# Kernel optimization log

Hardware: AMD Instinct MI355X
Metric: run time of the kernel (lower is better)

## Reference

```python
import jax, jax.numpy as jnp
import numpy as np

BN_EPS = 1e-5

def _binarize(x):
    # sign with STE semantics (Binarize on .data in torch => identity grad)
    b = jnp.where(x >= 0, 1.0, -1.0).astype(x.dtype)
    return x + jax.lax.stop_gradient(b - x)

def _bin_linear(x, w, b, binarize_input):
    xb = _binarize(x) if binarize_input else x
    wb = _binarize(w)
    return xb @ wb.T + b

def _bn(x, g, be, m, v):
    return (x - m) * (g * jax.lax.rsqrt(v + BN_EPS)) + be

def _hardtanh(x):
    return jnp.clip(x, -1.0, 1.0)

def setup_inputs() -> dict:
    key = jax.random.key(0)
    ks = jax.random.split(key, 8)
    B, D_in, H, D_out = 16384, 784, 4096, 10
    inp = {
        'x':  jax.random.normal(ks[0], (B, D_in), jnp.float32),
        'w1': jax.random.normal(ks[1], (H, D_in), jnp.float32) * 0.05,
        'b1': jax.random.normal(ks[2], (H,), jnp.float32) * 0.05,
        'g1': jnp.ones((H,), jnp.float32), 'be1': jnp.zeros((H,), jnp.float32),
        'm1': jnp.zeros((H,), jnp.float32), 'v1': jnp.ones((H,), jnp.float32),
        'w2': jax.random.normal(ks[3], (H, H), jnp.float32) * 0.05,
        'b2': jax.random.normal(ks[4], (H,), jnp.float32) * 0.05,
        'g2': jnp.ones((H,), jnp.float32), 'be2': jnp.zeros((H,), jnp.float32),
        'm2': jnp.zeros((H,), jnp.float32), 'v2': jnp.ones((H,), jnp.float32),
        'w3': jax.random.normal(ks[5], (H, H), jnp.float32) * 0.05,
        'b3': jax.random.normal(ks[6], (H,), jnp.float32) * 0.05,
        'g3': jnp.ones((H,), jnp.float32), 'be3': jnp.zeros((H,), jnp.float32),
        'm3': jnp.zeros((H,), jnp.float32), 'v3': jnp.ones((H,), jnp.float32),
        'w4': jax.random.normal(ks[7], (D_out, H), jnp.float32) * 0.05,
        'b4': jnp.zeros((D_out,), jnp.float32),
    }
    return inp

def reference(x, w1, b1, g1, be1, m1, v1,
              w2, b2, g2, be2, m2, v2,
              w3, b3, g3, be3, m3, v3,
              w4, b4):
    # eval mode: BN uses running stats, dropout is identity
    h = _bin_linear(x.reshape(-1, w1.shape[1]), w1, b1, binarize_input=False)
    h = _hardtanh(_bn(h, g1, be1, m1, v1))
    h = _bin_linear(h, w2, b2, binarize_input=True)
    h = _hardtanh(_bn(h, g2, be2, m2, v2))
    h = _bin_linear(h, w3, b3, binarize_input=True)
    h = _hardtanh(_bn(h, g3, be3, m3, v3))
    h = _bin_linear(h, w4, b4, binarize_input=True)
    return jax.nn.log_softmax(h, axis=1)
```

## Files before the change

kernel.cpp:

```cpp
#include <hip/hip_runtime.h>
#include <hip/hip_bf16.h>
#include <stdint.h>
#include <math.h>

#define BATCH 16384
#define DIN   784
#define HID   4096
#define DOUT  10
#define KW    128
#define KP    1600
#define CAP   1048576
#define BN_EPS 1e-5
#define TAU   0.05f

constexpr size_t SZ_BITS   = (size_t)BATCH * KW * 4;
constexpr size_t OFF_BITS1 = 0;
constexpr size_t OFF_BITS2 = OFF_BITS1 + SZ_BITS;
constexpr size_t OFF_W2B   = OFF_BITS2 + SZ_BITS;
constexpr size_t OFF_W3B   = OFF_W2B + (size_t)HID * KW * 4;
constexpr size_t OFF_W4B   = OFF_W3B + (size_t)HID * KW * 4;
constexpr size_t OFF_CNT   = OFF_W4B + 8192;
constexpr size_t OFF_LIST  = OFF_CNT + 256;
constexpr size_t OFF_XHL   = (OFF_LIST + (size_t)CAP * 4 + 255) & ~(size_t)255;
constexpr size_t OFF_WSD   = OFF_XHL + (size_t)BATCH * KP * 2;

typedef __attribute__((ext_vector_type(8))) short frag8;
typedef __attribute__((ext_vector_type(4))) float f32x4;

typedef const __attribute__((address_space(1))) uint32_t guint;
typedef __attribute__((address_space(3))) uint32_t luint;

__device__ __forceinline__ void load16_to_lds(const void* g, void* l) {
  __builtin_amdgcn_global_load_lds((guint*)g, (luint*)l, 16, 0, 0);
}

__device__ __forceinline__ unsigned short f2bf_bits(float x) {
  __hip_bfloat16 h = __float2bfloat16(x);
  return *reinterpret_cast<unsigned short*>(&h);
}
__device__ __forceinline__ float bf2f(unsigned short b) {
  union { unsigned int u; float f; } c;
  c.u = ((unsigned int)b) << 16;
  return c.f;
}

__global__ void zero_cnt_kernel(int* cnt) {
  if (threadIdx.x == 0) *cnt = 0;
}

__global__ __launch_bounds__(256) void binarize_kernel(
    const float* __restrict__ w, uint32_t* __restrict__ bits, int nwords) {
  int t = blockIdx.x * 256 + threadIdx.x;
  if (t >= nwords) return;
  const float* p = w + (size_t)t * 32;
  uint32_t word = 0;
#pragma unroll
  for (int q = 0; q < 8; ++q) {
    float4 v = *(const float4*)(p + q * 4);
    word |= (uint32_t)(v.x >= 0.f) << (4 * q + 0);
    word |= (uint32_t)(v.y >= 0.f) << (4 * q + 1);
    word |= (uint32_t)(v.z >= 0.f) << (4 * q + 2);
    word |= (uint32_t)(v.w >= 0.f) << (4 * q + 3);
  }
  bits[t] = word;
}

__global__ __launch_bounds__(256) void convert_x_kernel(
    const float* __restrict__ X, short* __restrict__ Xhl) {
  int idx = blockIdx.x * 256 + threadIdx.x;
  int row = idx / 50, kq = idx - row * 50;
  short* orow = Xhl + (size_t)row * KP;
  if (kq < 49) {
    const float* p = X + (size_t)row * DIN + kq * 16;
    short hi[16], lo[16];
#pragma unroll
    for (int q = 0; q < 4; ++q) {
      float4 v = *(const float4*)(p + q * 4);
      float vv[4] = {v.x, v.y, v.z, v.w};
#pragma unroll
      for (int e = 0; e < 4; ++e) {
        unsigned short h = f2bf_bits(vv[e]);
        hi[q * 4 + e] = (short)h;
        lo[q * 4 + e] = (short)f2bf_bits(vv[e] - bf2f(h));
      }
    }
    *(uint4*)(orow + kq * 16)           = *(uint4*)&hi[0];
    *(uint4*)(orow + kq * 16 + 8)       = *(uint4*)&hi[8];
    *(uint4*)(orow + 784 + kq * 16)     = *(uint4*)&lo[0];
    *(uint4*)(orow + 784 + kq * 16 + 8) = *(uint4*)&lo[8];
  } else {
    uint4 z = {0, 0, 0, 0};
#pragma unroll
    for (int q = 0; q < 4; ++q) *(uint4*)(orow + 1568 + q * 8) = z;
  }
}

__global__ __launch_bounds__(256) void convert_w_kernel(
    const float* __restrict__ W, short* __restrict__ Wsd) {
  int idx = blockIdx.x * 256 + threadIdx.x;
  int row = idx / 50, kq = idx - row * 50;
  short* orow = Wsd + (size_t)row * KP;
  if (kq < 49) {
    const float* p = W + (size_t)row * DIN + kq * 16;
    short s[16];
#pragma unroll
    for (int q = 0; q < 4; ++q) {
      float4 v = *(const float4*)(p + q * 4);
      s[q * 4 + 0] = (short)((v.x >= 0.f) ? 0x3F80 : 0xBF80);
      s[q * 4 + 1] = (short)((v.y >= 0.f) ? 0x3F80 : 0xBF80);
      s[q * 4 + 2] = (short)((v.z >= 0.f) ? 0x3F80 : 0xBF80);
      s[q * 4 + 3] = (short)((v.w >= 0.f) ? 0x3F80 : 0xBF80);
    }
    *(uint4*)(orow + kq * 16)           = *(uint4*)&s[0];
    *(uint4*)(orow + kq * 16 + 8)       = *(uint4*)&s[8];
    *(uint4*)(orow + 784 + kq * 16)     = *(uint4*)&s[0];
    *(uint4*)(orow + 784 + kq * 16 + 8) = *(uint4*)&s[8];
  } else {
    uint4 z = {0, 0, 0, 0};
#pragma unroll
    for (int q = 0; q < 4; ++q) *(uint4*)(orow + 1568 + q * 8) = z;
  }
}

__global__ __launch_bounds__(256) void gemm1_mfma_kernel(
    const short* __restrict__ Xhl, const short* __restrict__ Wsd,
    const float* __restrict__ Bv, const float* __restrict__ Gv,
    const float* __restrict__ BEv, const float* __restrict__ Mv,
    const float* __restrict__ Vv,
    uint32_t* __restrict__ bits_out, int* __restrict__ cnt,
    uint32_t* __restrict__ list) {
  __shared__ short Ah[128 * 64];
  __shared__ short Bh[128 * 64];
  __shared__ unsigned short PW16[128 * 8];

  const int tid = threadIdx.x;
  const int bid = blockIdx.x;
  const int grp = bid >> 10;
  const int rem = bid & 1023;
  const int cb  = (grp << 3) + (rem & 7);
  const int rb  = rem >> 3;
  const int m0 = rb * 128, n0 = cb * 128;

  const int lane = tid & 63;
  const int w  = tid >> 6;
  const int wm = w & 1;
  const int wn = w >> 1;
  const int l15 = lane & 15;
  const int l4  = lane >> 4;

  f32x4 acc[4][4];
#pragma unroll
  for (int i = 0; i < 4; ++i)
#pragma unroll
    for (int j = 0; j < 4; ++j) acc[i][j] = (f32x4){0.f, 0.f, 0.f, 0.f};

  const int srow = lane >> 3;
  const int schunk = (lane & 7) ^ srow;
  const char* gA = (const char*)(Xhl + (size_t)(m0 + w * 32) * KP)
                   + (size_t)srow * (KP * 2) + schunk * 16;
  const char* gB = (const char*)(Wsd + (size_t)(n0 + w * 32) * KP)
                   + (size_t)srow * (KP * 2) + schunk * 16;
  short* ldsA = &Ah[(w * 32) * 64];
  short* ldsB = &Bh[(w * 32) * 64];

  for (int s = 0; s < 25; ++s) {
#pragma unroll
    for (int rr = 0; rr < 4; ++rr) {
      load16_to_lds(gA + (size_t)rr * 8 * KP * 2, ldsA + rr * 8 * 64);
      load16_to_lds(gB + (size_t)rr * 8 * KP * 2, ldsB + rr * 8 * 64);
    }
    gA += 128;  gB += 128;
    __syncthreads();
#pragma unroll
    for (int h = 0; h < 2; ++h) {
      frag8 af[4], bf[4];
#pragma unroll
      for (int f = 0; f < 4; ++f) {
        const int ma = wm * 64 + f * 16 + l15;
        const int nb = wn * 64 + f * 16 + l15;
        const int ca = ((h * 4 + l4) ^ (l15 & 7)) * 8;
        af[f] = *(const frag8*)&Ah[ma * 64 + ca];
        bf[f] = *(const frag8*)&Bh[nb * 64 + ca];
      }
#pragma unroll
      for (int fm = 0; fm < 4; ++fm)
#pragma unroll
        for (int fn = 0; fn < 4; ++fn)
          acc[fm][fn] = __builtin_amdgcn_mfma_f32_16x16x32_bf16(
              af[fm], bf[fn], acc[fm][fn], 0, 0, 0);
    }
    __syncthreads();
  }

#pragma unroll
  for (int fn = 0; fn < 4; ++fn) {
    const int gj = n0 + wn * 64 + fn * 16 + l15;
    const float  bj = Bv[gj];
    const double scale = (double)Gv[gj] / sqrt((double)Vv[gj] + BN_EPS);
    const double mj = (double)Mv[gj], bej = (double)BEv[gj];
    const double thr = (double)TAU * fabs(scale);
#pragma unroll
    for (int fm = 0; fm < 4; ++fm) {
#pragma unroll
      for (int r = 0; r < 4; ++r) {
        const int row_l = wm * 64 + fm * 16 + l4 * 4 + r;
        float hb = acc[fm][fn][r] + bj;
        double bnd = ((double)hb - mj) * scale + bej;
        unsigned int bit = (bnd >= 0.0) ? 1u : 0u;
        unsigned long long mask = __ballot(bit);
        if (l15 == 0)
          PW16[row_l * 8 + (wn * 4 + fn)] =
              (unsigned short)(mask >> (l4 * 16));
        if (fabs(bnd) < thr) {
          int pos = atomicAdd(cnt, 1);
          if (pos < CAP)
            list[pos] = (uint32_t)((m0 + row_l) * HID + gj);
        }
      }
    }
  }
  __syncthreads();
  for (int t = tid; t < 512; t += 256) {
    int row = t >> 2, wc = t & 3;
    uint32_t word = (uint32_t)PW16[row * 8 + wc * 2] |
                    ((uint32_t)PW16[row * 8 + wc * 2 + 1] << 16);
    bits_out[(size_t)(m0 + row) * KW + (n0 >> 5) + wc] = word;
  }
}

__global__ __launch_bounds__(256) void fixup_chain_kernel(
    const float* __restrict__ X, const float* __restrict__ W,
    const float* __restrict__ Bv, const float* __restrict__ Gv,
    const float* __restrict__ BEv, const float* __restrict__ Mv,
    const float* __restrict__ Vv,
    uint32_t* __restrict__ bits1, const int* __restrict__ cnt,
    const uint32_t* __restrict__ list) {
  int n = *cnt;
  if (n > CAP) n = CAP;
  for (int idx = blockIdx.x * 256 + threadIdx.x; idx < n;
       idx += gridDim.x * 256) {
    uint32_t code = list[idx];
    int i = code >> 12;
    int j = code & (HID - 1);
    const float* xr = X + (size_t)i * DIN;
    const float* wr = W + (size_t)j * DIN;
    float h = 0.f;
    for (int k = 0; k < DIN; k += 4) {
      float4 xv = *(const float4*)(xr + k);
      float4 wv = *(const float4*)(wr + k);
      h = fmaf(xv.x, (wv.x >= 0.f) ? 1.f : -1.f, h);
      h = fmaf(xv.y, (wv.y >= 0.f) ? 1.f : -1.f, h);
      h = fmaf(xv.z, (wv.z >= 0.f) ? 1.f : -1.f, h);
      h = fmaf(xv.w, (wv.w >= 0.f) ? 1.f : -1.f, h);
    }
    float hb = h + Bv[j];
    double scale = (double)Gv[j] / sqrt((double)Vv[j] + BN_EPS);
    double bnd = ((double)hb - (double)Mv[j]) * scale + (double)BEv[j];
    uint32_t bit = (bnd >= 0.0) ? 1u : 0u;
    uint32_t* wpw = &bits1[(size_t)i * KW + (j >> 5)];
    uint32_t cur = (*wpw >> (j & 31)) & 1u;
    if (cur != bit) atomicXor(wpw, 1u << (j & 31));
  }
}

__global__ __launch_bounds__(256) void bitgemm_kernel(
    const uint32_t* __restrict__ Abits, const uint32_t* __restrict__ Wbits,
    const float* __restrict__ Bv, const float* __restrict__ Gv,
    const float* __restrict__ BEv, const float* __restrict__ Mv,
    const float* __restrict__ Vv, uint32_t* __restrict__ bits_out) {
  __shared__ uint32_t As[16 * 128];
  __shared__ uint32_t Bs[16 * 128];
  __shared__ unsigned int PW[128 * 4];

  const int tid = threadIdx.x;
  const int cb = blockIdx.x & 31, rb = blockIdx.x >> 5;
  const int m0 = rb * 128, n0 = cb * 128;
  const int tx = tid & 15, ty = tid >> 4;

  int acc[8][8];
#pragma unroll
  for (int r = 0; r < 8; ++r)
#pragma unroll
    for (int c = 0; c < 8; ++c) acc[r][c] = 0;

  const int sr = tid >> 1;
  const int sk = (tid & 1) * 8;
  const uint32_t* arow = Abits + (size_t)(m0 + sr) * KW + sk;
  const uint32_t* wrow = Wbits + (size_t)(n0 + sr) * KW + sk;

  for (int w0 = 0; w0 < KW; w0 += 16) {
    uint4 a0 = *(const uint4*)(arow + w0);
    uint4 a1 = *(const uint4*)(arow + w0 + 4);
    uint4 b0 = *(const uint4*)(wrow + w0);
    uint4 b1 = *(const uint4*)(wrow + w0 + 4);
    __syncthreads();
    As[(sk + 0) * 128 + sr] = a0.x;  As[(sk + 1) * 128 + sr] = a0.y;
    As[(sk + 2) * 128 + sr] = a0.z;  As[(sk + 3) * 128 + sr] = a0.w;
    As[(sk + 4) * 128 + sr] = a1.x;  As[(sk + 5) * 128 + sr] = a1.y;
    As[(sk + 6) * 128 + sr] = a1.z;  As[(sk + 7) * 128 + sr] = a1.w;
    Bs[(sk + 0) * 128 + sr] = b0.x;  Bs[(sk + 1) * 128 + sr] = b0.y;
    Bs[(sk + 2) * 128 + sr] = b0.z;  Bs[(sk + 3) * 128 + sr] = b0.w;
    Bs[(sk + 4) * 128 + sr] = b1.x;  Bs[(sk + 5) * 128 + sr] = b1.y;
    Bs[(sk + 6) * 128 + sr] = b1.z;  Bs[(sk + 7) * 128 + sr] = b1.w;
    __syncthreads();
#pragma unroll
    for (int kk = 0; kk < 16; ++kk) {
      uint32_t a[8], b[8];
      *(uint4*)&a[0] = *(const uint4*)&As[kk * 128 + ty * 8];
      *(uint4*)&a[4] = *(const uint4*)&As[kk * 128 + ty * 8 + 4];
      *(uint4*)&b[0] = *(const uint4*)&Bs[kk * 128 + tx * 8];
      *(uint4*)&b[4] = *(const uint4*)&Bs[kk * 128 + tx * 8 + 4];
#pragma unroll
      for (int r = 0; r < 8; ++r)
#pragma unroll
        for (int c = 0; c < 8; ++c)
          acc[r][c] += __popc(a[r] ^ b[c]);
    }
  }

  uint32_t bm[8];
#pragma unroll
  for (int r = 0; r < 8; ++r) bm[r] = 0;
  for (int c = 0; c < 8; ++c) {
    const int j = n0 + tx * 8 + c;
    const double scale = (double)Gv[j] / sqrt((double)Vv[j] + BN_EPS);
    const double mj = (double)Mv[j], bej = (double)BEv[j], bj = (double)Bv[j];
#pragma unroll
    for (int r = 0; r < 8; ++r) {
      double h = (double)(HID - 2 * acc[r][c]) + bj;
      double bnd = (h - mj) * scale + bej;
      bm[r] |= (uint32_t)(bnd >= 0.0) << c;
    }
  }
  for (int t = tid; t < 512; t += 256) PW[t] = 0u;
  __syncthreads();
#pragma unroll
  for (int r = 0; r < 8; ++r)
    atomicOr(&PW[(ty * 8 + r) * 4 + (tx >> 2)], bm[r] << (8 * (tx & 3)));
  __syncthreads();
  for (int w = tid; w < 512; w += 256) {
    int row = w >> 2, wc = w & 3;
    bits_out[(size_t)(m0 + row) * KW + (n0 >> 5) + wc] = PW[row * 4 + wc];
  }
}

__global__ __launch_bounds__(256) void final_kernel(
    const uint32_t* __restrict__ xbits, const uint32_t* __restrict__ w4b,
    const float* __restrict__ b4, float* __restrict__ out) {
  __shared__ uint32_t Ws[DOUT * KW];
  const int tid = threadIdx.x;
  for (int t = tid; t < DOUT * KW; t += 256) Ws[t] = w4b[t];
  __syncthreads();
  const int lane = tid & 63;
  const int i = blockIdx.x * 4 + (tid >> 6);
  const uint32_t x0 = xbits[(size_t)i * KW + lane];
  const uint32_t x1 = xbits[(size_t)i * KW + 64 + lane];
  int cnt[DOUT];
#pragma unroll
  for (int j = 0; j < DOUT; ++j)
    cnt[j] = __popc(x0 ^ Ws[j * KW + lane]) + __popc(x1 ^ Ws[j * KW + 64 + lane]);
#pragma unroll
  for (int j = 0; j < DOUT; ++j)
#pragma unroll
    for (int off = 32; off; off >>= 1) cnt[j] += __shfl_xor(cnt[j], off);
  double logit[DOUT];
  double mx = -1e300;
#pragma unroll
  for (int j = 0; j < DOUT; ++j) {
    logit[j] = (double)(HID - 2 * cnt[j]) + (double)b4[j];
    mx = fmax(mx, logit[j]);
  }
  double s = 0.0;
#pragma unroll
  for (int j = 0; j < DOUT; ++j) s += exp(logit[j] - mx);
  double lse = log(s) + mx;
  if (lane < DOUT)
    out[(size_t)i * DOUT + lane] = (float)(logit[lane] - lse);
}

extern "C" void kernel_launch(void* const* d_in, const int* in_sizes, int n_in,
                              void* d_out, int out_size, void* d_ws, size_t ws_size,
                              hipStream_t stream) {
  const float* x   = (const float*)d_in[0];
  const float* w1  = (const float*)d_in[1];
  const float* b1  = (const float*)d_in[2];
  const float* g1  = (const float*)d_in[3];
  const float* be1 = (const float*)d_in[4];
  const float* m1  = (const float*)d_in[5];
  const float* v1  = (const float*)d_in[6];
  const float* w2  = (const float*)d_in[7];
  const float* b2  = (const float*)d_in[8];
  const float* g2  = (const float*)d_in[9];
  const float* be2 = (const float*)d_in[10];
  const float* m2  = (const float*)d_in[11];
  const float* v2  = (const float*)d_in[12];
  const float* w3  = (const float*)d_in[13];
  const float* b3  = (const float*)d_in[14];
  const float* g3  = (const float*)d_in[15];
  const float* be3 = (const float*)d_in[16];
  const float* m3  = (const float*)d_in[17];
  const float* v3  = (const float*)d_in[18];
  const float* w4  = (const float*)d_in[19];
  const float* b4  = (const float*)d_in[20];

  char* ws = (char*)d_ws;
  uint32_t* bits1 = (uint32_t*)(ws + OFF_BITS1);
  uint32_t* bits2 = (uint32_t*)(ws + OFF_BITS2);
  uint32_t* w2b   = (uint32_t*)(ws + OFF_W2B);
  uint32_t* w3b   = (uint32_t*)(ws + OFF_W3B);
  uint32_t* w4b   = (uint32_t*)(ws + OFF_W4B);
  int*      cnt   = (int*)(ws + OFF_CNT);
  uint32_t* list  = (uint32_t*)(ws + OFF_LIST);
  short*    xhl   = (short*)(ws + OFF_XHL);
  short*    wsd   = (short*)(ws + OFF_WSD);
  float*    out   = (float*)d_out;

  zero_cnt_kernel<<<1, 64, 0, stream>>>(cnt);
  binarize_kernel<<<(HID * KW + 255) / 256, 256, 0, stream>>>(w2, w2b, HID * KW);
  binarize_kernel<<<(HID * KW + 255) / 256, 256, 0, stream>>>(w3, w3b, HID * KW);
  binarize_kernel<<<(DOUT * KW + 255) / 256, 256, 0, stream>>>(w4, w4b, DOUT * KW);
  convert_x_kernel<<<(BATCH * 50) / 256, 256, 0, stream>>>(x, xhl);
  convert_w_kernel<<<(HID * 50) / 256, 256, 0, stream>>>(w1, wsd);

  gemm1_mfma_kernel<<<(BATCH / 128) * (HID / 128), 256, 0, stream>>>(
      xhl, wsd, b1, g1, be1, m1, v1, bits1, cnt, list);
  fixup_chain_kernel<<<512, 256, 0, stream>>>(
      x, w1, b1, g1, be1, m1, v1, bits1, cnt, list);

  bitgemm_kernel<<<(BATCH / 128) * (HID / 128), 256, 0, stream>>>(
      bits1, w2b, b2, g2, be2, m2, v2, bits2);
  bitgemm_kernel<<<(BATCH / 128) * (HID / 128), 256, 0, stream>>>(
      bits2, w3b, b3, g3, be3, m3, v3, bits1);

  final_kernel<<<BATCH / 4, 256, 0, stream>>>(bits1, w4b, b4, out);
}
```

Measured before the change: 2.502 ms.

## Feed gemm1 from bit-packed W1 expanded in registers, drop LDS staging

Replaces the bf16 sign-expanded W1 copy with a bit-packed W1, one byte per 8 signs, which is expanded into bf16 ±1 MFMA fragments in registers. GEMM1 now reads A and B fragments directly from global memory without LDS staging. The tile widens to 128x256 with 32 accumulators per wave. Both GEMM kernels also get an XCD-aware block-to-tile mapping for L2 locality. The intent is to cut W1 conversion traffic and LDS/sync overhead, at the cost of uncoalesced direct global loads, higher register pressure and ALU work for sign expansion.

Measured after the change: 2.665 ms. 6.5% more time.

```diff
diff --git a/kernel.cpp b/kernel.cpp
--- a/kernel.cpp
+++ b/kernel.cpp
@@ -19,20 +19,13 @@
 constexpr size_t OFF_W2B   = OFF_BITS2 + SZ_BITS;
 constexpr size_t OFF_W3B   = OFF_W2B + (size_t)HID * KW * 4;
 constexpr size_t OFF_W4B   = OFF_W3B + (size_t)HID * KW * 4;
-constexpr size_t OFF_CNT   = OFF_W4B + 8192;
+constexpr size_t OFF_W1B   = OFF_W4B + 8192;
+constexpr size_t OFF_CNT   = OFF_W1B + (size_t)HID * 128;
 constexpr size_t OFF_LIST  = OFF_CNT + 256;
 constexpr size_t OFF_XHL   = (OFF_LIST + (size_t)CAP * 4 + 255) & ~(size_t)255;
-constexpr size_t OFF_WSD   = OFF_XHL + (size_t)BATCH * KP * 2;
 
 typedef __attribute__((ext_vector_type(8))) short frag8;
 typedef __attribute__((ext_vector_type(4))) float f32x4;
-
-typedef const __attribute__((address_space(1))) uint32_t guint;
-typedef __attribute__((address_space(3))) uint32_t luint;
-
-__device__ __forceinline__ void load16_to_lds(const void* g, void* l) {
-  __builtin_amdgcn_global_load_lds((guint*)g, (luint*)l, 16, 0, 0);
-}
 
 __device__ __forceinline__ unsigned short f2bf_bits(float x) {
   __hip_bfloat16 h = __float2bfloat16(x);
@@ -42,6 +35,16 @@
   union { unsigned int u; float f; } c;
   c.u = ((unsigned int)b) << 16;
   return c.f;
+}
+
+__device__ __forceinline__ frag8 expand_signs(uint32_t wb) {
+  uint32_t nw = ~wb;
+  union { uint32_t u[4]; frag8 f; } r;
+#pragma unroll
+  for (int j = 0; j < 4; ++j)
+    r.u[j] = 0x3F803F80u | (((nw >> (2 * j)) & 1u) << 15)
+                         | (((nw >> (2 * j + 1)) & 1u) << 31);
+  return r.f;
 }
 
 __global__ void zero_cnt_kernel(int* cnt) {
@@ -63,6 +66,20 @@
     word |= (uint32_t)(v.w >= 0.f) << (4 * q + 3);
   }
   bits[t] = word;
+}
+
+__global__ __launch_bounds__(256) void binarize_w1_kernel(
+    const float* __restrict__ w, uint32_t* __restrict__ bits) {
+  int idx = blockIdx.x * 256 + threadIdx.x;
+  if (idx >= HID * 25) return;
+  int row = idx / 25, wq = idx - row * 25;
+  int kbase = wq * 32;
+  int nv = (kbase + 32 <= DIN) ? 32 : (DIN - kbase);
+  const float* p = w + (size_t)row * DIN + kbase;
+  uint32_t word = 0;
+  for (int e = 0; e < nv; ++e)
+    word |= (uint32_t)(p[e] >= 0.f) << e;
+  bits[(size_t)row * 32 + wq] = word;
 }
 
 __global__ __launch_bounds__(256) void convert_x_kernel(
@@ -95,122 +112,95 @@
   }
 }
 
-__global__ __launch_bounds__(256) void convert_w_kernel(
-    const float* __restrict__ W, short* __restrict__ Wsd) {
-  int idx = blockIdx.x * 256 + threadIdx.x;
-  int row = idx / 50, kq = idx - row * 50;
-  short* orow = Wsd + (size_t)row * KP;
-  if (kq < 49) {
-    const float* p = W + (size_t)row * DIN + kq * 16;
-    short s[16];
-#pragma unroll
-    for (int q = 0; q < 4; ++q) {
-      float4 v = *(const float4*)(p + q * 4);
-      s[q * 4 + 0] = (short)((v.x >= 0.f) ? 0x3F80 : 0xBF80);
-      s[q * 4 + 1] = (short)((v.y >= 0.f) ? 0x3F80 : 0xBF80);
-      s[q * 4 + 2] = (short)((v.z >= 0.f) ? 0x3F80 : 0xBF80);
-      s[q * 4 + 3] = (short)((v.w >= 0.f) ? 0x3F80 : 0xBF80);
-    }
-    *(uint4*)(orow + kq * 16)           = *(uint4*)&s[0];
-    *(uint4*)(orow + kq * 16 + 8)       = *(uint4*)&s[8];
-    *(uint4*)(orow + 784 + kq * 16)     = *(uint4*)&s[0];
-    *(uint4*)(orow + 784 + kq * 16 + 8) = *(uint4*)&s[8];
-  } else {
-    uint4 z = {0, 0, 0, 0};
-#pragma unroll
-    for (int q = 0; q < 4; ++q) *(uint4*)(orow + 1568 + q * 8) = z;
-  }
-}
-
 __global__ __launch_bounds__(256) void gemm1_mfma_kernel(
-    const short* __restrict__ Xhl, const short* __restrict__ Wsd,
+    const short* __restrict__ Xhl, const uint8_t* __restrict__ W1b,
     const float* __restrict__ Bv, const float* __restrict__ Gv,
     const float* __restrict__ BEv, const float* __restrict__ Mv,
     const float* __restrict__ Vv,
     uint32_t* __restrict__ bits_out, int* __restrict__ cnt,
     uint32_t* __restrict__ list) {
-  __shared__ short Ah[128 * 64];
-  __shared__ short Bh[128 * 64];
-  __shared__ unsigned short PW16[128 * 8];
+  __shared__ unsigned short PW16[128 * 16];
 
   const int tid = threadIdx.x;
   const int bid = blockIdx.x;
-  const int grp = bid >> 10;
-  const int rem = bid & 1023;
-  const int cb  = (grp << 3) + (rem & 7);
-  const int rb  = rem >> 3;
-  const int m0 = rb * 128, n0 = cb * 128;
+  const int xcd = bid & 7;
+  const int t   = bid >> 3;
+  const int cb  = t & 15;
+  const int rb  = xcd * 16 + (t >> 4);
+  const int m0 = rb * 128, n0 = cb * 256;
 
   const int lane = tid & 63;
-  const int w  = tid >> 6;
-  const int wm = w & 1;
-  const int wn = w >> 1;
-  const int l15 = lane & 15;
-  const int l4  = lane >> 4;
-
-  f32x4 acc[4][4];
+  const int wv = tid >> 6;
+  const int wm = wv & 1, wn = wv >> 1;
+  const int l15 = lane & 15, l4 = lane >> 4;
+
+  f32x4 acc[4][8];
 #pragma unroll
   for (int i = 0; i < 4; ++i)
 #pragma unroll
-    for (int j = 0; j < 4; ++j) acc[i][j] = (f32x4){0.f, 0.f, 0.f, 0.f};
-
-  const int srow = lane >> 3;
-  const int schunk = (lane & 7) ^ srow;
-  const char* gA = (const char*)(Xhl + (size_t)(m0 + w * 32) * KP)
-                   + (size_t)srow * (KP * 2) + schunk * 16;
-  const char* gB = (const char*)(Wsd + (size_t)(n0 + w * 32) * KP)
-                   + (size_t)srow * (KP * 2) + schunk * 16;
-  short* ldsA = &Ah[(w * 32) * 64];
-  short* ldsB = &Bh[(w * 32) * 64];
+    for (int j = 0; j < 8; ++j) acc[i][j] = (f32x4){0.f, 0.f, 0.f, 0.f};
+
+  const short* arow[4];
+#pragma unroll
+  for (int mf = 0; mf < 4; ++mf)
+    arow[mf] = Xhl + (size_t)(m0 + wm * 64 + mf * 16 + l15) * KP;
+  const uint8_t* brow[8];
+#pragma unroll
+  for (int nf = 0; nf < 8; ++nf)
+    brow[nf] = W1b + (size_t)(n0 + wn * 128 + nf * 16 + l15) * 128;
 
   for (int s = 0; s < 25; ++s) {
-#pragma unroll
-    for (int rr = 0; rr < 4; ++rr) {
-      load16_to_lds(gA + (size_t)rr * 8 * KP * 2, ldsA + rr * 8 * 64);
-      load16_to_lds(gB + (size_t)rr * 8 * KP * 2, ldsB + rr * 8 * 64);
-    }
-    gA += 128;  gB += 128;
-    __syncthreads();
+    int bo[2];
 #pragma unroll
     for (int h = 0; h < 2; ++h) {
-      frag8 af[4], bf[4];
-#pragma unroll
-      for (int f = 0; f < 4; ++f) {
-        const int ma = wm * 64 + f * 16 + l15;
-        const int nb = wn * 64 + f * 16 + l15;
-        const int ca = ((h * 4 + l4) ^ (l15 & 7)) * 8;
-        af[f] = *(const frag8*)&Ah[ma * 64 + ca];
-        bf[f] = *(const frag8*)&Bh[nb * 64 + ca];
-      }
-#pragma unroll
-      for (int fm = 0; fm < 4; ++fm)
-#pragma unroll
-        for (int fn = 0; fn < 4; ++fn)
-          acc[fm][fn] = __builtin_amdgcn_mfma_f32_16x16x32_bf16(
-              af[fm], bf[fn], acc[fm][fn], 0, 0, 0);
-    }
-    __syncthreads();
-  }
-
-#pragma unroll
-  for (int fn = 0; fn < 4; ++fn) {
-    const int gj = n0 + wn * 64 + fn * 16 + l15;
+      int kg = s * 64 + h * 32 + l4 * 8;
+      int k2 = (kg >= 1568) ? 0 : (kg >= 784 ? kg - 784 : kg);
+      bo[h] = k2 >> 3;
+    }
+    uint32_t wb[2][8];
+#pragma unroll
+    for (int h = 0; h < 2; ++h)
+#pragma unroll
+      for (int nf = 0; nf < 8; ++nf)
+        wb[h][nf] = brow[nf][bo[h]];
+    frag8 af[4][2];
+#pragma unroll
+    for (int mf = 0; mf < 4; ++mf)
+#pragma unroll
+      for (int h = 0; h < 2; ++h)
+        af[mf][h] = *(const frag8*)(arow[mf] + s * 64 + h * 32 + l4 * 8);
+#pragma unroll
+    for (int h = 0; h < 2; ++h) {
+      frag8 bf[8];
+#pragma unroll
+      for (int nf = 0; nf < 8; ++nf) bf[nf] = expand_signs(wb[h][nf]);
+#pragma unroll
+      for (int mf = 0; mf < 4; ++mf)
+#pragma unroll
+        for (int nf = 0; nf < 8; ++nf)
+          acc[mf][nf] = __builtin_amdgcn_mfma_f32_16x16x32_bf16(
+              af[mf][h], bf[nf], acc[mf][nf], 0, 0, 0);
+    }
+  }
+
+#pragma unroll
+  for (int nf = 0; nf < 8; ++nf) {
+    const int gj = n0 + wn * 128 + nf * 16 + l15;
     const float  bj = Bv[gj];
     const double scale = (double)Gv[gj] / sqrt((double)Vv[gj] + BN_EPS);
     const double mj = (double)Mv[gj], bej = (double)BEv[gj];
     const double thr = (double)TAU * fabs(scale);
 #pragma unroll
-    for (int fm = 0; fm < 4; ++fm) {
+    for (int mf = 0; mf < 4; ++mf) {
 #pragma unroll
       for (int r = 0; r < 4; ++r) {
-        const int row_l = wm * 64 + fm * 16 + l4 * 4 + r;
-        float hb = acc[fm][fn][r] + bj;
+        const int row_l = wm * 64 + mf * 16 + l4 * 4 + r;
+        float hb = acc[mf][nf][r] + bj;
         double bnd = ((double)hb - mj) * scale + bej;
         unsigned int bit = (bnd >= 0.0) ? 1u : 0u;
         unsigned long long mask = __ballot(bit);
         if (l15 == 0)
-          PW16[row_l * 8 + (wn * 4 + fn)] =
-              (unsigned short)(mask >> (l4 * 16));
+          PW16[row_l * 16 + wn * 8 + nf] = (unsigned short)(mask >> (l4 * 16));
         if (fabs(bnd) < thr) {
           int pos = atomicAdd(cnt, 1);
           if (pos < CAP)
@@ -220,11 +210,11 @@
     }
   }
   __syncthreads();
-  for (int t = tid; t < 512; t += 256) {
-    int row = t >> 2, wc = t & 3;
-    uint32_t word = (uint32_t)PW16[row * 8 + wc * 2] |
-                    ((uint32_t)PW16[row * 8 + wc * 2 + 1] << 16);
-    bits_out[(size_t)(m0 + row) * KW + (n0 >> 5) + wc] = word;
+  for (int t2 = tid; t2 < 1024; t2 += 256) {
+    int row = t2 >> 3, wc = t2 & 7;
+    uint32_t word = (uint32_t)PW16[row * 16 + wc * 2] |
+                    ((uint32_t)PW16[row * 16 + wc * 2 + 1] << 16);
+    bits_out[(size_t)(m0 + row) * KW + cb * 8 + wc] = word;
   }
 }
 
@@ -273,7 +263,11 @@
   __shared__ unsigned int PW[128 * 4];
 
   const int tid = threadIdx.x;
-  const int cb = blockIdx.x & 31, rb = blockIdx.x >> 5;
+  const int bid = blockIdx.x;
+  const int xcd = bid & 7;
+  const int t   = bid >> 3;
+  const int cb  = t & 31;
+  const int rb  = xcd * 16 + (t >> 5);
   const int m0 = rb * 128, n0 = cb * 128;
   const int tx = tid & 15, ty = tid >> 4;
 
@@ -332,7 +326,7 @@
       bm[r] |= (uint32_t)(bnd >= 0.0) << c;
     }
   }
-  for (int t = tid; t < 512; t += 256) PW[t] = 0u;
+  for (int t2 = tid; t2 < 512; t2 += 256) PW[t2] = 0u;
   __syncthreads();
 #pragma unroll
   for (int r = 0; r < 8; ++r)
@@ -409,21 +403,21 @@
   uint32_t* w2b   = (uint32_t*)(ws + OFF_W2B);
   uint32_t* w3b   = (uint32_t*)(ws + OFF_W3B);
   uint32_t* w4b   = (uint32_t*)(ws + OFF_W4B);
+  uint32_t* w1b   = (uint32_t*)(ws + OFF_W1B);
   int*      cnt   = (int*)(ws + OFF_CNT);
   uint32_t* list  = (uint32_t*)(ws + OFF_LIST);
   short*    xhl   = (short*)(ws + OFF_XHL);
-  short*    wsd   = (short*)(ws + OFF_WSD);
   float*    out   = (float*)d_out;
 
   zero_cnt_kernel<<<1, 64, 0, stream>>>(cnt);
   binarize_kernel<<<(HID * KW + 255) / 256, 256, 0, stream>>>(w2, w2b, HID * KW);
   binarize_kernel<<<(HID * KW + 255) / 256, 256, 0, stream>>>(w3, w3b, HID * KW);
   binarize_kernel<<<(DOUT * KW + 255) / 256, 256, 0, stream>>>(w4, w4b, DOUT * KW);
+  binarize_w1_kernel<<<(HID * 25 + 255) / 256, 256, 0, stream>>>(w1, w1b);
   convert_x_kernel<<<(BATCH * 50) / 256, 256, 0, stream>>>(x, xhl);
-  convert_w_kernel<<<(HID * 50) / 256, 256, 0, stream>>>(w1, wsd);
-
-  gemm1_mfma_kernel<<<(BATCH / 128) * (HID / 128), 256, 0, stream>>>(
-      xhl, wsd, b1, g1, be1, m1, v1, bits1, cnt, list);
+
+  gemm1_mfma_kernel<<<(BATCH / 128) * (HID / 256), 256, 0, stream>>>(
+      xhl, (const uint8_t*)w1b, b1, g1, be1, m1, v1, bits1, cnt, list);
   fixup_chain_kernel<<<512, 256, 0, stream>>>(
       x, w1, b1, g1, be1, m1, v1, bits1, cnt, list);
 
```
